# Optimization experiments

Hardware: AMD Instinct MI355X
Metric: run time of the kernel (lower is better)

The kernel has to match this reference:

```python
import jax, jax.numpy as jnp
import numpy as np


def setup_inputs() -> dict:
    key = jax.random.key(0)
    ks = jax.random.split(key, 9)
    B, C, H, W = 4, 256, 64, 64
    Ci = C // 2
    s = 0.05  # keep activations numerically tame
    return {
        "x": jax.random.normal(ks[0], (B, C, H, W), jnp.float32),
        "w_g": jax.random.normal(ks[1], (Ci, C), jnp.float32) * s,
        "b_g": jax.random.normal(ks[2], (Ci,), jnp.float32) * s,
        "w_theta": jax.random.normal(ks[3], (Ci, C), jnp.float32) * s,
        "b_theta": jax.random.normal(ks[4], (Ci,), jnp.float32) * s,
        "w_phi": jax.random.normal(ks[5], (Ci, C), jnp.float32) * s,
        "b_phi": jax.random.normal(ks[6], (Ci,), jnp.float32) * s,
        "w_out": jax.random.normal(ks[7], (C, Ci), jnp.float32) * s,
        "b_out": jax.random.normal(ks[8], (C,), jnp.float32) * s,
    }


def reference(x, w_g, b_g, w_theta, b_theta, w_phi, b_phi, w_out, b_out):
    B, C, H, W = x.shape
    Ci = w_g.shape[0]
    N = H * W
    xr = x.reshape(B, C, N)  # flatten spatial dims

    def proj(w, b):  # 1x1 conv == per-pixel GEMM
        return jnp.einsum("oc,bcn->bon", w, xr) + b[None, :, None]

    g_x = proj(w_g, b_g)          # [B, Ci, N]
    theta_x = proj(w_theta, b_theta)
    phi_x = proj(w_phi, b_phi)

    scale = jnp.asarray(Ci, x.dtype) ** 0.5
    f = jnp.einsum("bci,bcj->bij", theta_x, phi_x) / scale  # [B, N, N]
    attn = jax.nn.softmax(f, axis=-1)

    # out[b,c,i] = sum_j g_x[b,c,j] * attn[b,i,j]
    out = jnp.einsum("bcj,bij->bci", g_x, attn)             # [B, Ci, N]
    y = jnp.einsum("oc,bcn->bon", w_out, out) + b_out[None, :, None]
    return y.reshape(B, C, H, W) + x
```

## Files before the change

### kernel.cpp

```cpp
#include <hip/hip_runtime.h>
#include <hip/hip_bf16.h>


typedef float f32x4 __attribute__((ext_vector_type(4)));
typedef float f32x16 __attribute__((ext_vector_type(16)));
typedef short s16x8 __attribute__((ext_vector_type(8)));
typedef short s16x4 __attribute__((ext_vector_type(4)));

#define B_  4
#define C_  256
#define CI_ 128
#define N_  4096

#define OFF_Q    (8ull  << 20)
#define OFF_K    (12ull << 20)
#define OFF_G    (16ull << 20)
#define OFF_O    (20ull << 20)
#define OFF_WQK  (24ull << 20)
#define OFF_WG   (OFF_WQK + 131072)
#define OFF_WOUT (OFF_WG  + 65536)
#define OFF_BQK  (OFF_WOUT + 65536)
#define OFF_BG   (OFF_BQK + 1024)
#define OFF_BOUT (OFF_BG  + 512)
#define OFF_END  (OFF_BOUT + 1024)

__device__ inline f32x4 mfma16(s16x8 a, s16x8 b, f32x4 c) {
    return __builtin_amdgcn_mfma_f32_16x16x32_bf16(a, b, c, 0, 0, 0);
}
__device__ inline f32x16 mfma32(s16x8 a, s16x8 b, f32x16 c) {
    return __builtin_amdgcn_mfma_f32_32x32x16_bf16(a, b, c, 0, 0, 0);
}
__device__ inline s16x8 ld8(const __hip_bfloat16* p) { return *(const s16x8*)p; }
__device__ inline float b2f(short u) {
    return __uint_as_float(((unsigned int)(unsigned short)u) << 16);
}
__device__ inline unsigned int pk2(float a, float b) {
    __hip_bfloat162 h;
    h.x = __float2bfloat16(a); h.y = __float2bfloat16(b);
    return *(unsigned int*)&h;
}
__device__ inline void gload_lds16(const void* g, void* l) {
    __builtin_amdgcn_global_load_lds(
        (const __attribute__((address_space(1))) unsigned int*)g,
        (__attribute__((address_space(3))) unsigned int*)l, 16, 0, 0);
}
__device__ inline float fexp2(float x) { return __builtin_amdgcn_exp2f(x); }

__global__ void prep_weights(const float* wg, const float* bg,
                             const float* wt, const float* bt,
                             const float* wp, const float* bp,
                             const float* wo, const float* bo, char* ws) {
    __hip_bfloat16* Wqk  = (__hip_bfloat16*)(ws + OFF_WQK);
    __hip_bfloat16* Wg   = (__hip_bfloat16*)(ws + OFF_WG);
    __hip_bfloat16* Wout = (__hip_bfloat16*)(ws + OFF_WOUT);
    float* Bqk  = (float*)(ws + OFF_BQK);
    float* Bg   = (float*)(ws + OFF_BG);
    float* Bout = (float*)(ws + OFF_BOUT);
    const float rs = 0.08838834764831845f * 1.4426950408889634f;
    int idx = blockIdx.x * 256 + threadIdx.x;
    if (idx < 65536) {
        int r = idx >> 8, c = idx & 255;
        float v = (r < 128) ? wt[r * 256 + c] * rs : wp[(r - 128) * 256 + c];
        Wqk[idx] = __float2bfloat16(v);
    }
    if (idx < 32768) {
        Wg[idx]   = __float2bfloat16(wg[idx]);
        Wout[idx] = __float2bfloat16(wo[idx]);
    }
    if (idx < 256) { Bqk[idx] = (idx < 128) ? bt[idx] * rs : bp[idx - 128]; Bout[idx] = bo[idx]; }
    if (idx < 128) Bg[idx] = bg[idx];
}

__global__ __launch_bounds__(256) void proj(const float* x, char* ws) {
    const __hip_bfloat16* Wqk = (const __hip_bfloat16*)(ws + OFF_WQK);
    const __hip_bfloat16* Wg  = (const __hip_bfloat16*)(ws + OFF_WG);
    const float* Bqk = (const float*)(ws + OFF_BQK);
    const float* Bg  = (const float*)(ws + OFF_BG);
    __hip_bfloat16* Q  = (__hip_bfloat16*)(ws + OFF_Q);
    __hip_bfloat16* Kb = (__hip_bfloat16*)(ws + OFF_K);
    __hip_bfloat16* G  = (__hip_bfloat16*)(ws + OFF_G);

    __shared__ char at[32 * 512];

    int b = blockIdx.y, n0 = blockIdx.x * 32;
    int t = threadIdx.x;
    int w = t >> 6, l = t & 63, lr = l & 15, lg = l >> 4;

    {
        int n4 = (t & 7) * 4;
        int cp = t >> 3;
        const float* xb = x + ((size_t)b * C_) * N_ + n0 + n4;
#pragma unroll
        for (int p = 0; p < 4; p++) {
            int c0 = (p * 32 + cp) * 2;
            f32x4 vA = *(const f32x4*)(xb + (size_t)c0 * N_);
            f32x4 vB = *(const f32x4*)(xb + (size_t)(c0 + 1) * N_);
            int slot = c0 >> 3, coff = (c0 & 7) << 1;
#pragma unroll
            for (int i = 0; i < 4; i++) {
                int n = n4 + i;
                *(unsigned int*)(&at[n * 512 + ((slot ^ (n & 7)) << 4) + coff]) =
                    pk2(vA[i], vB[i]);
            }
        }
    }
    __syncthreads();

    f32x4 acc[4][2] = {};
    f32x4 accg[2][2] = {};
    int o0q = w * 64, o0g = w * 32;
#pragma unroll
    for (int kk = 0; kk < 8; kk++) {
        s16x8 a[2];
#pragma unroll
        for (int nf = 0; nf < 2; nf++) {
            int row = nf * 16 + lr;
            int s = (4 * kk + lg) ^ (row & 7);
            a[nf] = *(const s16x8*)(&at[row * 512 + s * 16]);
        }
#pragma unroll
        for (int of = 0; of < 4; of++) {
            s16x8 bb = ld8(Wqk + (size_t)(o0q + 16 * of + lr) * C_ + kk * 32 + lg * 8);
            acc[of][0] = mfma16(a[0], bb, acc[of][0]);
            acc[of][1] = mfma16(a[1], bb, acc[of][1]);
        }
#pragma unroll
        for (int og = 0; og < 2; og++) {
            s16x8 ag = ld8(Wg + (size_t)(o0g + 16 * og + lr) * C_ + kk * 32 + lg * 8);
            accg[og][0] = mfma16(ag, a[0], accg[og][0]);
            accg[og][1] = mfma16(ag, a[1], accg[og][1]);
        }
    }
#pragma unroll
    for (int of = 0; of < 4; of++) {
        int o = o0q + 16 * of + lr;
        float bias = Bqk[o];
#pragma unroll
        for (int nf = 0; nf < 2; nf++) {
#pragma unroll
            for (int i = 0; i < 4; i++) {
                int n = n0 + 16 * nf + lg * 4 + i;
                float v = acc[of][nf][i] + bias;
                if (o < 128) Q [(size_t)(b * N_ + n) * CI_ + o]         = __float2bfloat16(v);
                else         Kb[(size_t)(b * N_ + n) * CI_ + (o - 128)] = __float2bfloat16(v);
            }
        }
    }
#pragma unroll
    for (int og = 0; og < 2; og++) {
#pragma unroll
        for (int i = 0; i < 4; i++) {
            int o = o0g + 16 * og + lg * 4 + i;
            float bias = Bg[o];
#pragma unroll
            for (int nf = 0; nf < 2; nf++) {
                int n = n0 + 16 * nf + lr;
                G[(size_t)(b * CI_ + o) * N_ + n] = __float2bfloat16(accg[og][nf][i] + bias);
            }
        }
    }
}

__global__ __launch_bounds__(256, 3) void flash11(char* ws, int nchunk,
                                                  unsigned long long off_part,
                                                  unsigned long long off_ml) {
    const __hip_bfloat16* Q  = (const __hip_bfloat16*)(ws + OFF_Q);
    const __hip_bfloat16* Kb = (const __hip_bfloat16*)(ws + OFF_K);
    const __hip_bfloat16* G  = (const __hip_bfloat16*)(ws + OFF_G);
    __hip_bfloat16* OP = (__hip_bfloat16*)(ws + off_part);
    float* ML = (float*)(ws + off_ml);

    __shared__ char kbuf[2][32 * 256];
    __shared__ char vbuf[2][128 * 64];

    int L = blockIdx.x;
    int npairs = B_ * nchunk;
    int pair = L % npairs, qt = L / npairs;
    int b = pair / nchunk, cz = pair % nchunk;
    int per = 128 / nchunk, rem = 128 % nchunk;
    int jb_t = per * cz + (cz < rem ? cz : rem);
    int sz_t = per + (cz < rem ? 1 : 0);
    int jb = jb_t << 5, je = jb + (sz_t << 5);

    int w = threadIdx.x >> 6, l = threadIdx.x & 63;
    int cl = l & 31, hi = l >> 5;
    int q0 = qt * 128 + w * 32;
    int kkey = (l & 7) << 4;
    int vkey = (l >> 1) & 3;

    auto STAGE = [&](int pb_, int j0_) {
#pragma unroll
        for (int i = 0; i < 2; i++) {
            int row = w * 8 + i * 4 + (l >> 4);
            int bcol = ((l & 15) << 4) ^ ((row & 7) << 4);
            const char* src = (const char*)Kb + (((size_t)b * N_ + j0_ + row) << 8) + bcol;
            gload_lds16(src, &kbuf[pb_][(w * 8 + i * 4) * 256]);
        }
#pragma unroll
        for (int i = 0; i < 2; i++) {
            int c = w * 32 + i * 16 + (l >> 2);
            int srcslot = (l & 3) ^ ((l >> 3) & 3);
            const char* src = (const char*)G + ((((size_t)b * CI_ + c) * N_ + j0_) << 1)
                              + (srcslot << 4);
            gload_lds16(src, &vbuf[pb_][(w * 32 + i * 16) * 64]);
        }
    };

    s16x8 qb[8];
    {
        const __hip_bfloat16* qrow = Q + ((size_t)b * N_ + q0 + cl) * CI_ + hi * 8;
#pragma unroll
        for (int st = 0; st < 8; st++) qb[st] = ld8(qrow + st * 16);
    }

    f32x16 oacc[4] = {};
    float m_i = 0.f, lsum = 0.f;

    STAGE(0, jb);
    __syncthreads();
    int pb = 0;

    for (int j0 = jb; j0 < je; j0 += 32) {
        if (j0 + 32 < je) STAGE(pb ^ 1, j0 + 32);
        const char* kb = kbuf[pb];
        const char* vbb = vbuf[pb];
        f32x16 sa = {}, sb = {};
        __builtin_amdgcn_s_setprio(1);
#pragma unroll
        for (int st = 0; st < 4; st++) {
            s16x8 kfa = *(const s16x8*)(kb + cl * 256 + ((((st << 1) + hi) << 4) ^ kkey));
            s16x8 kfb = *(const s16x8*)(kb + cl * 256 + (((((st + 4) << 1) + hi) << 4) ^ kkey));
            sa = mfma32(kfa, qb[st], sa);
            sb = mfma32(kfb, qb[st + 4], sb);
        }
        __builtin_amdgcn_s_setprio(0);
        f32x16 s = sa + sb;
        if (j0 == jb) {
            float t0 = fmaxf(fmaxf(s[0], s[1]), fmaxf(s[2], s[3]));
            float t1 = fmaxf(fmaxf(s[4], s[5]), fmaxf(s[6], s[7]));
            float t2 = fmaxf(fmaxf(s[8], s[9]), fmaxf(s[10], s[11]));
            float t3 = fmaxf(fmaxf(s[12], s[13]), fmaxf(s[14], s[15]));
            float tm = fmaxf(fmaxf(t0, t1), fmaxf(t2, t3));
            tm = fmaxf(tm, __shfl_xor(tm, 32));
            m_i = tm;
        }
#pragma unroll
        for (int r = 0; r < 16; r++) s[r] = fexp2(s[r] - m_i);
        lsum += ((s[0] + s[1]) + (s[2] + s[3])) + ((s[4] + s[5]) + (s[6] + s[7]))
              + ((s[8] + s[9]) + (s[10] + s[11])) + ((s[12] + s[13]) + (s[14] + s[15]));
        union { unsigned int u[4]; s16x8 v; } pa0, pa1;
#pragma unroll
        for (int i = 0; i < 4; i++) {
            pa0.u[i] = pk2(s[2 * i], s[2 * i + 1]);
            pa1.u[i] = pk2(s[8 + 2 * i], s[9 + 2 * i]);
        }
        __builtin_amdgcn_s_setprio(1);
#pragma unroll
        for (int u = 0; u < 2; u++) {
            s16x8 pa = u ? pa1.v : pa0.v;
#pragma unroll
            for (int cb = 0; cb < 4; cb++) {
                const char* base = vbb + ((cb * 32 + cl) << 6) + hi * 8;
                union { s16x4 h[2]; s16x8 v; } vf;
                vf.h[0] = *(const s16x4*)(base + ((((u << 1))     ^ vkey) << 4));
                vf.h[1] = *(const s16x4*)(base + ((((u << 1) | 1) ^ vkey) << 4));
                oacc[cb] = mfma32(pa, vf.v, oacc[cb]);
            }
        }
        __builtin_amdgcn_s_setprio(0);
        __syncthreads();
        pb ^= 1;
    }
    lsum += __shfl_xor(lsum, 32);
#pragma unroll
    for (int cb = 0; cb < 4; cb++) {
#pragma unroll
        for (int r = 0; r < 16; r++) {
            int q = q0 + (r & 3) + 8 * (r >> 2) + 4 * hi;
            OP[((size_t)(cz * B_ + b) * N_ + q) * CI_ + cb * 32 + cl] =
                __float2bfloat16(oacc[cb][r]);
        }
    }
    if (l < 32) {
        size_t mi = ((size_t)(cz * B_ + b) * N_ + q0 + l) * 2;
        ML[mi] = m_i;
        ML[mi + 1] = lsum;
    }
}

template <int NC>
__global__ __launch_bounds__(256) void combine(char* ws,
                                               unsigned long long off_part,
                                               unsigned long long off_ml) {
    const __hip_bfloat16* OP = (const __hip_bfloat16*)(ws + off_part);
    const float* ML = (const float*)(ws + off_ml);
    __hip_bfloat16* O = (__hip_bfloat16*)(ws + OFF_O);
    int idx = blockIdx.x * 256 + threadIdx.x;
    int cg = idx & 15, n = (idx >> 4) & (N_ - 1), b = idx >> 16;
    float mz[NC], lz[NC], M = -1e30f;
#pragma unroll
    for (int z = 0; z < NC; z++) {
        size_t mi = ((size_t)(z * B_ + b) * N_ + n) * 2;
        mz[z] = ML[mi]; lz[z] = ML[mi + 1];
        M = fmaxf(M, mz[z]);
    }
    float Lsum = 0.f, wz[NC];
#pragma unroll
    for (int z = 0; z < NC; z++) { wz[z] = fexp2(mz[z] - M); Lsum += lz[z] * wz[z]; }
    float inv = 1.f / Lsum;
    float o[8] = {};
#pragma unroll
    for (int z = 0; z < NC; z++) {
        s16x8 v = ld8(OP + ((size_t)(z * B_ + b) * N_ + n) * CI_ + cg * 8);
        float wv = wz[z] * inv;
#pragma unroll
        for (int i = 0; i < 8; i++) o[i] += wv * b2f(v[i]);
    }
    s16x8 r;
#pragma unroll
    for (int i = 0; i < 8; i++) {
        __hip_bfloat16 h = __float2bfloat16(o[i]);
        r[i] = *(short*)&h;
    }
    *(s16x8*)(O + ((size_t)b * N_ + n) * CI_ + cg * 8) = r;
}

__global__ __launch_bounds__(256) void gemm_out(const float* x, char* ws, float* y) {
    const __hip_bfloat16* Ob = (const __hip_bfloat16*)(ws + OFF_O);
    const __hip_bfloat16* Wo = (const __hip_bfloat16*)(ws + OFF_WOUT);
    const float* Bout = (const float*)(ws + OFF_BOUT);
    int b = blockIdx.y;
    int w = threadIdx.x >> 6, l = threadIdx.x & 63, lr = l & 15, lg = l >> 4;
    int n0 = blockIdx.x * 32;
    int o0 = w * 64;
    f32x4 acc[4][2] = {};
#pragma unroll
    for (int kk = 0; kk < 4; kk++) {
        s16x8 bb[2];
#pragma unroll
        for (int nf = 0; nf < 2; nf++)
            bb[nf] = ld8(Ob + (size_t)(b * N_ + n0 + 16 * nf + lr) * CI_ + kk * 32 + lg * 8);
#pragma unroll
        for (int of = 0; of < 4; of++) {
            s16x8 a = ld8(Wo + (size_t)(o0 + 16 * of + lr) * CI_ + kk * 32 + lg * 8);
#pragma unroll
            for (int nf = 0; nf < 2; nf++)
                acc[of][nf] = mfma16(a, bb[nf], acc[of][nf]);
        }
    }
#pragma unroll
    for (int of = 0; of < 4; of++) {
#pragma unroll
        for (int i = 0; i < 4; i++) {
            int o = o0 + 16 * of + lg * 4 + i;
            float bias = Bout[o];
#pragma unroll
            for (int nf = 0; nf < 2; nf++) {
                int n = n0 + 16 * nf + lr;
                size_t idx = (size_t)(b * C_ + o) * N_ + n;
                y[idx] = acc[of][nf][i] + bias + x[idx];
            }
        }
    }
}

extern "C" void kernel_launch(void* const* d_in, const int* in_sizes, int n_in,
                              void* d_out, int out_size, void* d_ws, size_t ws_size,
                              hipStream_t stream) {
    const float* x  = (const float*)d_in[0];
    const float* wg = (const float*)d_in[1];
    const float* bg = (const float*)d_in[2];
    const float* wt = (const float*)d_in[3];
    const float* bt = (const float*)d_in[4];
    const float* wp = (const float*)d_in[5];
    const float* bp = (const float*)d_in[6];
    const float* wo = (const float*)d_in[7];
    const float* bo = (const float*)d_in[8];
    char* ws = (char*)d_ws;
    float* y = (float*)d_out;

    unsigned long long need6 = OFF_END + (24ull << 20) + (1ull << 20);
    unsigned long long need4 = OFF_END + (16ull << 20) + (1ull << 20);
    int nchunk;
    unsigned long long off_part, off_ml;
    if (ws_size >= need6) {
        nchunk = 6; off_part = OFF_END; off_ml = OFF_END + (24ull << 20);
    } else if (ws_size >= need4) {
        nchunk = 4; off_part = OFF_END; off_ml = OFF_END + (16ull << 20);
    } else {
        nchunk = 2; off_part = 0ull; off_ml = OFF_END;
    }

    prep_weights<<<256, 256, 0, stream>>>(wg, bg, wt, bt, wp, bp, wo, bo, ws);
    proj<<<dim3(128, 4), 256, 0, stream>>>(x, ws);
    flash11<<<dim3(32 * B_ * nchunk), 256, 0, stream>>>(ws, nchunk, off_part, off_ml);
    if (nchunk == 6)      combine<6><<<1024, 256, 0, stream>>>(ws, off_part, off_ml);
    else if (nchunk == 4) combine<4><<<1024, 256, 0, stream>>>(ws, off_part, off_ml);
    else                  combine<2><<<1024, 256, 0, stream>>>(ws, off_part, off_ml);
    gemm_out<<<dim3(128, 4), 256, 0, stream>>>(x, ws, y);
}
```

Measured before the change: 95.77 us.

## Fuse split-KV combine into output projection GEMM and use single MFMA accumulator chain

Merges the combine kernel, which merges per-chunk partial attention outputs, into the output 1x1-conv GEMM. The normalized O tile is staged in swizzled shared memory rather than written to and reread from a global bf16 buffer, which removes one launch and one global round trip. The block now covers 16 pixels, so the grid doubles. Separately, the QK^T loop now uses one serial MFMA accumulator chain instead of two independent chains plus an add, which lengthens the dependency chain.

```diff
diff --git a/kernel.cpp b/kernel.cpp
--- a/kernel.cpp
+++ b/kernel.cpp
@@ -15,7 +15,6 @@
 #define OFF_Q    (8ull  << 20)
 #define OFF_K    (12ull << 20)
 #define OFF_G    (16ull << 20)
-#define OFF_O    (20ull << 20)
 #define OFF_WQK  (24ull << 20)
 #define OFF_WG   (OFF_WQK + 131072)
 #define OFF_WOUT (OFF_WG  + 65536)
@@ -161,9 +160,9 @@
     }
 }
 
-__global__ __launch_bounds__(256, 3) void flash11(char* ws, int nchunk,
-                                                  unsigned long long off_part,
-                                                  unsigned long long off_ml) {
+__global__ __launch_bounds__(256, 3) void flash9(char* ws, int nchunk,
+                                                 unsigned long long off_part,
+                                                 unsigned long long off_ml) {
     const __hip_bfloat16* Q  = (const __hip_bfloat16*)(ws + OFF_Q);
     const __hip_bfloat16* Kb = (const __hip_bfloat16*)(ws + OFF_K);
     const __hip_bfloat16* G  = (const __hip_bfloat16*)(ws + OFF_G);
@@ -224,17 +223,14 @@
         if (j0 + 32 < je) STAGE(pb ^ 1, j0 + 32);
         const char* kb = kbuf[pb];
         const char* vbb = vbuf[pb];
-        f32x16 sa = {}, sb = {};
+        f32x16 s = {};
         __builtin_amdgcn_s_setprio(1);
 #pragma unroll
-        for (int st = 0; st < 4; st++) {
-            s16x8 kfa = *(const s16x8*)(kb + cl * 256 + ((((st << 1) + hi) << 4) ^ kkey));
-            s16x8 kfb = *(const s16x8*)(kb + cl * 256 + (((((st + 4) << 1) + hi) << 4) ^ kkey));
-            sa = mfma32(kfa, qb[st], sa);
-            sb = mfma32(kfb, qb[st + 4], sb);
+        for (int st = 0; st < 8; st++) {
+            s16x8 kf = *(const s16x8*)(kb + cl * 256 + ((((st << 1) + hi) << 4) ^ kkey));
+            s = mfma32(kf, qb[st], s);
         }
         __builtin_amdgcn_s_setprio(0);
-        f32x16 s = sa + sb;
         if (j0 == jb) {
             float t0 = fmaxf(fmaxf(s[0], s[1]), fmaxf(s[2], s[3]));
             float t1 = fmaxf(fmaxf(s[4], s[5]), fmaxf(s[6], s[7]));
@@ -289,63 +285,61 @@
 }
 
 template <int NC>
-__global__ __launch_bounds__(256) void combine(char* ws,
-                                               unsigned long long off_part,
-                                               unsigned long long off_ml) {
+__global__ __launch_bounds__(256) void out_fused2(const float* x, char* ws, float* y,
+                                                  unsigned long long off_part,
+                                                  unsigned long long off_ml) {
     const __hip_bfloat16* OP = (const __hip_bfloat16*)(ws + off_part);
     const float* ML = (const float*)(ws + off_ml);
-    __hip_bfloat16* O = (__hip_bfloat16*)(ws + OFF_O);
-    int idx = blockIdx.x * 256 + threadIdx.x;
-    int cg = idx & 15, n = (idx >> 4) & (N_ - 1), b = idx >> 16;
-    float mz[NC], lz[NC], M = -1e30f;
-#pragma unroll
-    for (int z = 0; z < NC; z++) {
-        size_t mi = ((size_t)(z * B_ + b) * N_ + n) * 2;
-        mz[z] = ML[mi]; lz[z] = ML[mi + 1];
-        M = fmaxf(M, mz[z]);
-    }
-    float Lsum = 0.f, wz[NC];
-#pragma unroll
-    for (int z = 0; z < NC; z++) { wz[z] = fexp2(mz[z] - M); Lsum += lz[z] * wz[z]; }
-    float inv = 1.f / Lsum;
-    float o[8] = {};
-#pragma unroll
-    for (int z = 0; z < NC; z++) {
-        s16x8 v = ld8(OP + ((size_t)(z * B_ + b) * N_ + n) * CI_ + cg * 8);
-        float wv = wz[z] * inv;
-#pragma unroll
-        for (int i = 0; i < 8; i++) o[i] += wv * b2f(v[i]);
-    }
-    s16x8 r;
-#pragma unroll
-    for (int i = 0; i < 8; i++) {
-        __hip_bfloat16 h = __float2bfloat16(o[i]);
-        r[i] = *(short*)&h;
-    }
-    *(s16x8*)(O + ((size_t)b * N_ + n) * CI_ + cg * 8) = r;
-}
-
-__global__ __launch_bounds__(256) void gemm_out(const float* x, char* ws, float* y) {
-    const __hip_bfloat16* Ob = (const __hip_bfloat16*)(ws + OFF_O);
     const __hip_bfloat16* Wo = (const __hip_bfloat16*)(ws + OFF_WOUT);
     const float* Bout = (const float*)(ws + OFF_BOUT);
+
+    __shared__ char oT[16 * 256];
+
     int b = blockIdx.y;
-    int w = threadIdx.x >> 6, l = threadIdx.x & 63, lr = l & 15, lg = l >> 4;
-    int n0 = blockIdx.x * 32;
+    int n0 = blockIdx.x * 16;
+    int t = threadIdx.x;
+
+    {
+        int nl = t >> 4;
+        int cg = t & 15;
+        int n = n0 + nl;
+        float mz[NC], lz[NC], M = -1e30f;
+#pragma unroll
+        for (int z = 0; z < NC; z++) {
+            size_t mi = ((size_t)(z * B_ + b) * N_ + n) * 2;
+            mz[z] = ML[mi]; lz[z] = ML[mi + 1];
+            M = fmaxf(M, mz[z]);
+        }
+        float Ls = 0.f, wz[NC];
+#pragma unroll
+        for (int z = 0; z < NC; z++) { wz[z] = fexp2(mz[z] - M); Ls += lz[z] * wz[z]; }
+        float inv = 1.f / Ls;
+        float o8[8] = {};
+#pragma unroll
+        for (int z = 0; z < NC; z++) {
+            s16x8 v = ld8(OP + ((size_t)(z * B_ + b) * N_ + n) * CI_ + cg * 8);
+            float wv = wz[z] * inv;
+#pragma unroll
+            for (int e = 0; e < 8; e++) o8[e] += wv * b2f(v[e]);
+        }
+        union { unsigned int u[4]; s16x8 v; } r;
+#pragma unroll
+        for (int e = 0; e < 4; e++) r.u[e] = pk2(o8[2 * e], o8[2 * e + 1]);
+        *(s16x8*)(&oT[nl * 256 + ((cg ^ (nl & 7)) << 4)]) = r.v;
+    }
+    __syncthreads();
+
+    int w = t >> 6, l = t & 63, lr = l & 15, lg = l >> 4;
     int o0 = w * 64;
-    f32x4 acc[4][2] = {};
+    f32x4 acc[4] = {};
 #pragma unroll
     for (int kk = 0; kk < 4; kk++) {
-        s16x8 bb[2];
-#pragma unroll
-        for (int nf = 0; nf < 2; nf++)
-            bb[nf] = ld8(Ob + (size_t)(b * N_ + n0 + 16 * nf + lr) * CI_ + kk * 32 + lg * 8);
+        int slot = kk * 4 + lg;
+        s16x8 bb = *(const s16x8*)(&oT[lr * 256 + ((slot ^ (lr & 7)) << 4)]);
 #pragma unroll
         for (int of = 0; of < 4; of++) {
             s16x8 a = ld8(Wo + (size_t)(o0 + 16 * of + lr) * CI_ + kk * 32 + lg * 8);
-#pragma unroll
-            for (int nf = 0; nf < 2; nf++)
-                acc[of][nf] = mfma16(a, bb[nf], acc[of][nf]);
+            acc[of] = mfma16(a, bb, acc[of]);
         }
     }
 #pragma unroll
@@ -353,13 +347,9 @@
 #pragma unroll
         for (int i = 0; i < 4; i++) {
             int o = o0 + 16 * of + lg * 4 + i;
-            float bias = Bout[o];
-#pragma unroll
-            for (int nf = 0; nf < 2; nf++) {
-                int n = n0 + 16 * nf + lr;
-                size_t idx = (size_t)(b * C_ + o) * N_ + n;
-                y[idx] = acc[of][nf][i] + bias + x[idx];
-            }
+            int n = n0 + lr;
+            size_t idx = (size_t)(b * C_ + o) * N_ + n;
+            y[idx] = acc[of][i] + Bout[o] + x[idx];
         }
     }
 }
@@ -393,9 +383,11 @@
 
     prep_weights<<<256, 256, 0, stream>>>(wg, bg, wt, bt, wp, bp, wo, bo, ws);
     proj<<<dim3(128, 4), 256, 0, stream>>>(x, ws);
-    flash11<<<dim3(32 * B_ * nchunk), 256, 0, stream>>>(ws, nchunk, off_part, off_ml);
-    if (nchunk == 6)      combine<6><<<1024, 256, 0, stream>>>(ws, off_part, off_ml);
-    else if (nchunk == 4) combine<4><<<1024, 256, 0, stream>>>(ws, off_part, off_ml);
-    else                  combine<2><<<1024, 256, 0, stream>>>(ws, off_part, off_ml);
-    gemm_out<<<dim3(128, 4), 256, 0, stream>>>(x, ws, y);
-}
+    flash9<<<dim3(32 * B_ * nchunk), 256, 0, stream>>>(ws, nchunk, off_part, off_ml);
+    if (nchunk == 6)
+        out_fused2<6><<<dim3(256, 4), 256, 0, stream>>>(x, ws, y, off_part, off_ml);
+    else if (nchunk == 4)
+        out_fused2<4><<<dim3(256, 4), 256, 0, stream>>>(x, ws, y, off_part, off_ml);
+    else
+        out_fused2<2><<<dim3(256, 4), 256, 0, stream>>>(x, ws, y, off_part, off_ml);
+}
```

Result: no change. 95.92 us (+0.2%).
